# Kernel tuning notes

Measured on AMD Instinct MI355X. Metric: run time of the kernel, lower is better.

Reference implementation:

```python
import jax, jax.numpy as jnp
import numpy as np

B, S, D, UNITS = 4, 2048, 4096, 4096

def setup_inputs() -> dict:
    key = jax.random.key(0)
    k1, k2 = jax.random.split(key)
    x = jax.random.normal(k1, (B, S, D), dtype=jnp.float32)
    # int8 quantized kernel, values in [-127, 127]
    quantized_kernel = jax.random.randint(k2, (D, UNITS), -127, 128, dtype=jnp.int32).astype(jnp.int8)
    scale = jnp.float32(0.02)
    return {"x": x, "quantized_kernel": quantized_kernel, "scale": scale}

def reference(x, quantized_kernel, scale):
    # Dequantize int8 weights to fp32 and apply linear transform: y = x @ (W_int8 * scale)
    kernel_fp32 = quantized_kernel.astype(jnp.float32) * scale
    return jnp.einsum("bsd,du->bsu", x, kernel_fp32)
```

## Files before the change

### kernel.cpp

```cpp
#include <hip/hip_runtime.h>
#include <cstdint>

typedef unsigned short u16;
typedef __bf16 bf16x8 __attribute__((ext_vector_type(8)));
typedef float f32x4 __attribute__((ext_vector_type(4)));
typedef int   i32x4 __attribute__((ext_vector_type(4)));
typedef u16   u16x4 __attribute__((ext_vector_type(4)));

#define M_DIM 8192
#define N_DIM 4096
#define K_DIM 4096

#define GLOBAL_AS(p) ((const __attribute__((address_space(1))) void*)(p))
#define LDS_AS(p)    ((__attribute__((address_space(3))) void*)(p))

__device__ __forceinline__ u16 f2bf(float f) {
    union { float f; uint32_t u; } x; x.f = f;
    uint32_t u = x.u;
    uint32_t r = (u + 0x7fffu + ((u >> 16) & 1u)) >> 16;
    return (u16)r;
}

__global__ __launch_bounds__(256) void prepass_kernel(const float* __restrict__ X,
                                                      const int* __restrict__ W,
                                                      u16* __restrict__ Xb,
                                                      u16* __restrict__ Wt) {
    const int bid = blockIdx.x;
    const int t   = threadIdx.x;
    if (bid < 4096) {
        __shared__ int tile[64][65];
        const int n0 = (bid & 63) * 64;
        const int k0 = (bid >> 6) * 64;
#pragma unroll
        for (int i = 0; i < 4; i++) {
            int e = t + i * 256;
            int r = e >> 4;
            int c = (e & 15) * 4;
            i32x4 v = __builtin_nontemporal_load(
                (const i32x4*)(W + (size_t)(k0 + r) * N_DIM + n0 + c));
            tile[r][c] = v.x; tile[r][c + 1] = v.y; tile[r][c + 2] = v.z; tile[r][c + 3] = v.w;
        }
        __syncthreads();
        {
            int n = t >> 2, ks = (t & 3) * 16;
            __align__(16) u16 o[16];
#pragma unroll
            for (int i = 0; i < 16; i++)
                o[i] = f2bf((float)tile[ks + i][n]);
            u16* dst = Wt + (size_t)(n0 + n) * K_DIM + k0 + ks;
            *(uint4*)(dst)     = *(const uint4*)&o[0];
            *(uint4*)(dst + 8) = *(const uint4*)&o[8];
        }
    } else {
        const size_t base = (size_t)(bid - 4096) * 4096;
        const f32x4*   x4 = (const f32x4*)X;
        u16x4*         o4 = (u16x4*)Xb;
#pragma unroll
        for (int it = 0; it < 8; it++) {
            size_t ia = base + (size_t)it * 512 + t;
            size_t ib = ia + 256;
            f32x4 a = __builtin_nontemporal_load(x4 + ia);
            f32x4 b = __builtin_nontemporal_load(x4 + ib);
            u16x4 oa, ob;
            oa.x = f2bf(a.x); oa.y = f2bf(a.y); oa.z = f2bf(a.z); oa.w = f2bf(a.w);
            ob.x = f2bf(b.x); ob.y = f2bf(b.y); ob.z = f2bf(b.z); ob.w = f2bf(b.w);
            o4[ia] = oa;
            o4[ib] = ob;
        }
    }
}

__global__ __launch_bounds__(256) void gemm_bf16_kernel(const u16* __restrict__ A,
                                                        const u16* __restrict__ Bt,
                                                        const float* __restrict__ scale_p,
                                                        float* __restrict__ C) {
    __shared__ u16 As[128 * 32];
    __shared__ u16 Bs[128 * 32];

    const int tid  = threadIdx.x;
    const int lane = tid & 63;
    const int wv   = tid >> 6;
    const int m0   = blockIdx.y * 128;
    const int n0   = blockIdx.x * 128;

    const int wm = (wv >> 1) * 64;
    const int wn = (wv & 1) * 64;
    const int fr = lane & 15;
    const int fk = (lane >> 4) * 8;

    const int c0 = tid, c1 = tid + 256;
    const u16* ga0 = A  + (size_t)(m0 + (c0 >> 2)) * K_DIM + (c0 & 3) * 8;
    const u16* ga1 = A  + (size_t)(m0 + (c1 >> 2)) * K_DIM + (c1 & 3) * 8;
    const u16* gb0 = Bt + (size_t)(n0 + (c0 >> 2)) * K_DIM + (c0 & 3) * 8;
    const u16* gb1 = Bt + (size_t)(n0 + (c1 >> 2)) * K_DIM + (c1 & 3) * 8;
    u16* lA0 = As + wv * 512;
    u16* lA1 = As + 2048 + wv * 512;
    u16* lB0 = Bs + wv * 512;
    u16* lB1 = Bs + 2048 + wv * 512;

    f32x4 acc[4][4] = {};

    for (int k0 = 0; k0 < K_DIM; k0 += 32) {
        __builtin_amdgcn_global_load_lds(GLOBAL_AS(ga0 + k0), LDS_AS(lA0), 16, 0, 0);
        __builtin_amdgcn_global_load_lds(GLOBAL_AS(ga1 + k0), LDS_AS(lA1), 16, 0, 0);
        __builtin_amdgcn_global_load_lds(GLOBAL_AS(gb0 + k0), LDS_AS(lB0), 16, 0, 0);
        __builtin_amdgcn_global_load_lds(GLOBAL_AS(gb1 + k0), LDS_AS(lB1), 16, 0, 0);
        __syncthreads();

        bf16x8 af[4], bfr[4];
#pragma unroll
        for (int i = 0; i < 4; i++)
            af[i] = *(const bf16x8*)(As + (wm + i * 16 + fr) * 32 + fk);
#pragma unroll
        for (int j = 0; j < 4; j++)
            bfr[j] = *(const bf16x8*)(Bs + (wn + j * 16 + fr) * 32 + fk);
#pragma unroll
        for (int i = 0; i < 4; i++)
#pragma unroll
            for (int j = 0; j < 4; j++)
                acc[i][j] = __builtin_amdgcn_mfma_f32_16x16x32_bf16(af[i], bfr[j], acc[i][j], 0, 0, 0);
        __syncthreads();
    }

    const float s = *scale_p;
    const int orow = m0 + wm + (lane >> 4) * 4;
    const int ocol = n0 + wn + (lane & 15);
#pragma unroll
    for (int i = 0; i < 4; i++)
#pragma unroll
        for (int j = 0; j < 4; j++) {
            float* cp = C + (size_t)(orow + i * 16) * N_DIM + ocol + j * 16;
#pragma unroll
            for (int r = 0; r < 4; r++)
                __builtin_nontemporal_store(acc[i][j][r] * s, cp + (size_t)r * N_DIM);
        }
}

__global__ __launch_bounds__(256) void fb_gemm_kernel(const float* __restrict__ X,
                                                      const int* __restrict__ W,
                                                      const float* __restrict__ sp,
                                                      float* __restrict__ Y) {
    __shared__ float Xs[16][64];
    __shared__ float Ws[16][64];
    const int t = threadIdx.x;
    const int tx = t & 15, ty = t >> 4;
    const int m0 = blockIdx.y * 64, n0 = blockIdx.x * 64;
    float acc[4][4] = {};
    for (int k0 = 0; k0 < K_DIM; k0 += 16) {
#pragma unroll
        for (int i = 0; i < 4; i++) {
            int e = t + i * 256;
            int r = e >> 4, c = e & 15;
            Xs[c][r] = X[(size_t)(m0 + r) * K_DIM + k0 + c];
            int rw = e >> 6, cw = e & 63;
            Ws[rw][cw] = (float)W[(size_t)(k0 + rw) * N_DIM + n0 + cw];
        }
        __syncthreads();
#pragma unroll
        for (int kk = 0; kk < 16; kk++)
#pragma unroll
            for (int i = 0; i < 4; i++)
#pragma unroll
                for (int j = 0; j < 4; j++)
                    acc[i][j] += Xs[kk][ty * 4 + i] * Ws[kk][tx * 4 + j];
        __syncthreads();
    }
    const float s = *sp;
#pragma unroll
    for (int i = 0; i < 4; i++)
#pragma unroll
        for (int j = 0; j < 4; j++)
            Y[(size_t)(m0 + ty * 4 + i) * N_DIM + n0 + tx * 4 + j] = acc[i][j] * s;
}

extern "C" void kernel_launch(void* const* d_in, const int* in_sizes, int n_in,
                              void* d_out, int out_size, void* d_ws, size_t ws_size,
                              hipStream_t stream) {
    const float* X  = (const float*)d_in[0];
    const int*   W  = (const int*)d_in[1];
    const float* sp = (const float*)d_in[2];
    float* Y = (float*)d_out;

    const size_t xb = (size_t)M_DIM * K_DIM * sizeof(u16);
    const size_t wb = (size_t)N_DIM * K_DIM * sizeof(u16);

    if (ws_size >= xb + wb) {
        u16* Xb = (u16*)d_ws;
        u16* Wt = (u16*)((char*)d_ws + xb);
        prepass_kernel<<<6144, 256, 0, stream>>>(X, W, Xb, Wt);
        gemm_bf16_kernel<<<dim3(N_DIM / 128, M_DIM / 128), 256, 0, stream>>>(Xb, Wt, sp, Y);
    } else {
        fb_gemm_kernel<<<dim3(N_DIM / 64, M_DIM / 64), 256, 0, stream>>>(X, W, sp, Y);
    }
}
```

Baseline: 557.8 us.

## Rewrite bf16 GEMM as 256x256 double-buffered, swizzled, ping-pong pipelined kernel

```diff
diff --git a/kernel.cpp b/kernel.cpp
--- a/kernel.cpp
+++ b/kernel.cpp
@@ -70,70 +70,162 @@
     }
 }
 
-__global__ __launch_bounds__(256) void gemm_bf16_kernel(const u16* __restrict__ A,
-                                                        const u16* __restrict__ Bt,
-                                                        const float* __restrict__ scale_p,
-                                                        float* __restrict__ C) {
-    __shared__ u16 As[128 * 32];
-    __shared__ u16 Bs[128 * 32];
+
+#define BK 64
+#define NT (K_DIM / BK)
+static_assert(NT >= 4 && (NT & 1) == 0, "tile count must be even and >= 4");
+
+#define BARRIER() do { asm volatile("" ::: "memory"); \
+                       __builtin_amdgcn_s_barrier();  \
+                       asm volatile("" ::: "memory"); } while (0)
+#define WAIT_LGKM() asm volatile("s_waitcnt lgkmcnt(0)" ::: "memory")
+#define VMCNT(n)    asm volatile("s_waitcnt vmcnt(" #n ")" ::: "memory")
+
+#define READ_A(dst, mhv)                                                          \
+    _Pragma("unroll") for (int i = 0; i < 4; i++) {                               \
+        const char* p_ = As_ + ((mhv) * 128 + wrow * 64 + i * 16 + fr) * 128;     \
+        _Pragma("unroll") for (int kk = 0; kk < 2; kk++)                          \
+            dst[i][kk] = *(const bf16x8*)(p_ + ((kk * 64 + fk2) ^ sw));           \
+    }
+
+#define READ_B(dst, nhv)                                                          \
+    _Pragma("unroll") for (int j = 0; j < 2; j++) {                               \
+        const char* p_ = Bs_ + ((nhv) * 128 + wcol * 32 + j * 16 + fr) * 128;     \
+        _Pragma("unroll") for (int kk = 0; kk < 2; kk++)                          \
+            dst[j][kk] = *(const bf16x8*)(p_ + ((kk * 64 + fk2) ^ sw));           \
+    }
+
+#define MFMA_Q(MH, NH, aarr, barr)                                                \
+    do {                                                                          \
+        __builtin_amdgcn_s_setprio(1);                                            \
+        _Pragma("unroll") for (int kk = 0; kk < 2; kk++)                          \
+            _Pragma("unroll") for (int i = 0; i < 4; i++)                         \
+                _Pragma("unroll") for (int j = 0; j < 2; j++)                     \
+                    acc[MH][NH][i][j] = __builtin_amdgcn_mfma_f32_16x16x32_bf16(  \
+                        aarr[i][kk], barr[j][kk], acc[MH][NH][i][j], 0, 0, 0);    \
+        __builtin_amdgcn_s_setprio(0);                                            \
+    } while (0)
+
+#define STAGE_A(bufv, h, kt)                                                      \
+    do {                                                                          \
+        const u16* g_ = gA + (size_t)(h) * (128 * K_DIM) + (kt) * 64;             \
+        char* l_ = (char*)lds + (bufv) * 32768 + (h) * 16384 + wv * 1024;         \
+        __builtin_amdgcn_global_load_lds(GLOBAL_AS(g_ + aoff0), LDS_AS(l_), 16, 0, 0);        \
+        __builtin_amdgcn_global_load_lds(GLOBAL_AS(g_ + aoff1), LDS_AS(l_ + 8192), 16, 0, 0); \
+    } while (0)
+
+#define STAGE_B(bufv, h, kt)                                                      \
+    do {                                                                          \
+        const u16* g_ = gB + (size_t)(h) * (128 * K_DIM) + (kt) * 64;             \
+        char* l_ = (char*)lds + 65536 + (bufv) * 32768 + (h) * 16384 + wv * 1024; \
+        __builtin_amdgcn_global_load_lds(GLOBAL_AS(g_ + aoff0), LDS_AS(l_), 16, 0, 0);        \
+        __builtin_amdgcn_global_load_lds(GLOBAL_AS(g_ + aoff1), LDS_AS(l_ + 8192), 16, 0, 0); \
+    } while (0)
+
+#define TILE(bv, S1, S2, S3, S4, SYNC)                                            \
+    {                                                                             \
+        const char* As_ = (const char*)lds + (bv) * 32768;                        \
+        const char* Bs_ = (const char*)lds + 65536 + (bv) * 32768;                \
+        bf16x8 a0[4][2], a1[4][2], b0[2][2], b1[2][2];                            \
+                                                                         \
+        READ_A(a0, 0); READ_B(b0, 0);                                             \
+        S1;                                                                       \
+        BARRIER(); WAIT_LGKM();                                                   \
+        MFMA_Q(0, 0, a0, b0);                                                     \
+        BARRIER();                                                                \
+                                                                         \
+        READ_B(b1, 1);                                                            \
+        S2;                                                                       \
+        BARRIER(); WAIT_LGKM();                                                   \
+        MFMA_Q(0, 1, a0, b1);                                                     \
+        BARRIER();                                                                \
+                                                                         \
+        READ_A(a1, 1);                                                            \
+        S3;                                                                       \
+        BARRIER(); WAIT_LGKM();                                                   \
+        MFMA_Q(1, 0, a1, b0);                                                     \
+        BARRIER();                                                                \
+                                                                         \
+        S4;                                                                       \
+        BARRIER();                                                                \
+        MFMA_Q(1, 1, a1, b1);                                                     \
+        SYNC;                                                                     \
+        BARRIER();                                                                \
+    }
+
+__global__ __launch_bounds__(512, 2) void gemm_bf16_kernel(const u16* __restrict__ A,
+                                                           const u16* __restrict__ Bt,
+                                                           const float* __restrict__ scale_p,
+                                                           float* __restrict__ C) {
+    __shared__ __align__(16) u16 lds[65536];
 
     const int tid  = threadIdx.x;
     const int lane = tid & 63;
     const int wv   = tid >> 6;
-    const int m0   = blockIdx.y * 128;
-    const int n0   = blockIdx.x * 128;
-
-    const int wm = (wv >> 1) * 64;
-    const int wn = (wv & 1) * 64;
-    const int fr = lane & 15;
-    const int fk = (lane >> 4) * 8;
-
-    const int c0 = tid, c1 = tid + 256;
-    const u16* ga0 = A  + (size_t)(m0 + (c0 >> 2)) * K_DIM + (c0 & 3) * 8;
-    const u16* ga1 = A  + (size_t)(m0 + (c1 >> 2)) * K_DIM + (c1 & 3) * 8;
-    const u16* gb0 = Bt + (size_t)(n0 + (c0 >> 2)) * K_DIM + (c0 & 3) * 8;
-    const u16* gb1 = Bt + (size_t)(n0 + (c1 >> 2)) * K_DIM + (c1 & 3) * 8;
-    u16* lA0 = As + wv * 512;
-    u16* lA1 = As + 2048 + wv * 512;
-    u16* lB0 = Bs + wv * 512;
-    u16* lB1 = Bs + 2048 + wv * 512;
-
-    f32x4 acc[4][4] = {};
-
-    for (int k0 = 0; k0 < K_DIM; k0 += 32) {
-        __builtin_amdgcn_global_load_lds(GLOBAL_AS(ga0 + k0), LDS_AS(lA0), 16, 0, 0);
-        __builtin_amdgcn_global_load_lds(GLOBAL_AS(ga1 + k0), LDS_AS(lA1), 16, 0, 0);
-        __builtin_amdgcn_global_load_lds(GLOBAL_AS(gb0 + k0), LDS_AS(lB0), 16, 0, 0);
-        __builtin_amdgcn_global_load_lds(GLOBAL_AS(gb1 + k0), LDS_AS(lB1), 16, 0, 0);
-        __syncthreads();
-
-        bf16x8 af[4], bfr[4];
-#pragma unroll
-        for (int i = 0; i < 4; i++)
-            af[i] = *(const bf16x8*)(As + (wm + i * 16 + fr) * 32 + fk);
-#pragma unroll
-        for (int j = 0; j < 4; j++)
-            bfr[j] = *(const bf16x8*)(Bs + (wn + j * 16 + fr) * 32 + fk);
-#pragma unroll
-        for (int i = 0; i < 4; i++)
-#pragma unroll
-            for (int j = 0; j < 4; j++)
-                acc[i][j] = __builtin_amdgcn_mfma_f32_16x16x32_bf16(af[i], bfr[j], acc[i][j], 0, 0, 0);
-        __syncthreads();
-    }
+    const int wrow = wv >> 2;
+    const int wcol = wv & 3;
+
+    const int bid = blockIdx.x;
+    const int wg  = ((bid & 7) << 6) | (bid >> 3);
+    const size_t m0 = (size_t)(wg >> 4) * 256;
+    const size_t n0 = (size_t)(wg & 15) * 256;
+
+    const int fr  = lane & 15;
+    const int fk2 = (lane >> 4) * 16;
+    const int sw  = (lane & 7) << 4;
+
+    const int q0 = tid,       r0 = q0 >> 3, c0 = (q0 & 7) ^ (r0 & 7);
+    const int q1 = tid + 512, r1 = q1 >> 3, c1 = (q1 & 7) ^ (r1 & 7);
+    const size_t aoff0 = (size_t)r0 * K_DIM + c0 * 8;
+    const size_t aoff1 = (size_t)r1 * K_DIM + c1 * 8;
+
+    const u16* gA = A  + m0 * K_DIM;
+    const u16* gB = Bt + n0 * K_DIM;
+
+    f32x4 acc[2][2][4][2] = {};
+
+    STAGE_A(0, 0, 0);
+    STAGE_B(0, 0, 0);
+    STAGE_B(0, 1, 0);
+    STAGE_A(0, 1, 0);
+    STAGE_A(1, 0, 1);
+    STAGE_B(1, 0, 1);
+    STAGE_B(1, 1, 1);
+    VMCNT(6);
+    BARRIER();
+
+#pragma unroll 2
+    for (int T = 0; T < NT - 2; ++T) {
+        const int b  = T & 1;
+        const int bo = b ^ 1;
+        TILE(b,
+             STAGE_A(bo, 1, T + 1),
+             STAGE_A(b,  0, T + 2),
+             STAGE_B(b,  0, T + 2),
+             STAGE_B(b,  1, T + 2),
+             VMCNT(6));
+    }
+    TILE(0, STAGE_A(1, 1, NT - 1), , , , VMCNT(0));
+    TILE(1, , , , , );
 
     const float s = *scale_p;
-    const int orow = m0 + wm + (lane >> 4) * 4;
-    const int ocol = n0 + wn + (lane & 15);
-#pragma unroll
-    for (int i = 0; i < 4; i++)
-#pragma unroll
-        for (int j = 0; j < 4; j++) {
-            float* cp = C + (size_t)(orow + i * 16) * N_DIM + ocol + j * 16;
-#pragma unroll
-            for (int r = 0; r < 4; r++)
-                __builtin_nontemporal_store(acc[i][j][r] * s, cp + (size_t)r * N_DIM);
-        }
+    const int ec = lane & 15;
+    const int er = (lane >> 4) * 4;
+#pragma unroll
+    for (int mh = 0; mh < 2; mh++)
+#pragma unroll
+        for (int nh = 0; nh < 2; nh++)
+#pragma unroll
+            for (int i = 0; i < 4; i++)
+#pragma unroll
+                for (int j = 0; j < 2; j++) {
+                    float* cp = C + (m0 + mh * 128 + wrow * 64 + i * 16 + er) * N_DIM
+                                  + (n0 + nh * 128 + wcol * 32 + j * 16 + ec);
+#pragma unroll
+                    for (int r = 0; r < 4; r++)
+                        __builtin_nontemporal_store(acc[mh][nh][i][j][r] * s,
+                                                    cp + (size_t)r * N_DIM);
+                }
 }
 
 __global__ __launch_bounds__(256) void fb_gemm_kernel(const float* __restrict__ X,
@@ -188,7 +280,7 @@
         u16* Xb = (u16*)d_ws;
         u16* Wt = (u16*)((char*)d_ws + xb);
         prepass_kernel<<<6144, 256, 0, stream>>>(X, W, Xb, Wt);
-        gemm_bf16_kernel<<<dim3(N_DIM / 128, M_DIM / 128), 256, 0, stream>>>(Xb, Wt, sp, Y);
+        gemm_bf16_kernel<<<512, 512, 0, stream>>>(Xb, Wt, sp, Y);
     } else {
         fb_gemm_kernel<<<dim3(N_DIM / 64, M_DIM / 64), 256, 0, stream>>>(X, W, sp, Y);
     }
```

Result: faster. 470.3 us (-15.7%).
